# Performance work log

Measured on AMD Instinct MI355X. Metric: run time of the kernel, lower is better.

## Reference

```python
import jax, jax.numpy as jnp
import numpy as np

N_NODES = 50000
BN_EPS = 1e-5


def setup_inputs() -> dict:
    key = jax.random.key(0)
    ks = jax.random.split(key, 10)
    n, e, d, L = N_NODES, 500000, 128, 2
    x = jax.random.normal(ks[0], (n, d), dtype=jnp.float32)
    edge_index = jax.random.randint(ks[1], (2, e), 0, n, dtype=jnp.int64)
    edge_attr = jax.random.normal(ks[2], (e, d), dtype=jnp.float32)
    W1 = jax.random.normal(ks[3], (L, d, d), dtype=jnp.float32) * 0.05
    b1 = jax.random.normal(ks[4], (L, d), dtype=jnp.float32) * 0.02
    gamma = 1.0 + 0.1 * jax.random.normal(ks[5], (L, d), dtype=jnp.float32)
    beta = 0.1 * jax.random.normal(ks[6], (L, d), dtype=jnp.float32)
    W2 = jax.random.normal(ks[7], (L, d, d), dtype=jnp.float32) * 0.05
    b2 = jax.random.normal(ks[8], (L, d), dtype=jnp.float32) * 0.02
    return {"x": x, "edge_index": edge_index, "edge_attr": edge_attr,
            "W1": W1, "b1": b1, "gamma": gamma, "beta": beta, "W2": W2, "b2": b2}


def _gine_layer(x, src, dst, edge_attr, W1l, b1l, gl, bl, W2l, b2l):
    # GINEConv message: relu(x_j + edge_attr), sum-aggregated to target nodes
    msg = jax.nn.relu(x[src] + edge_attr)              # [E, d]
    agg = jax.ops.segment_sum(msg, dst, num_segments=N_NODES)  # [N, d]
    h = (x + agg) @ W1l + b1l                           # eps=0 -> (1+eps)*x = x
    # BatchNorm1d over nodes (train-mode batch stats, biased var)
    mu = jnp.mean(h, axis=0)
    var = jnp.mean(jnp.square(h - mu), axis=0)
    h = (h - mu) * jax.lax.rsqrt(var + BN_EPS) * gl + bl
    h = jax.nn.relu(h)
    h = jax.nn.relu(h @ W2l + b2l)
    return jax.nn.relu(h)  # encoder's outer activation


def reference(x, edge_index, edge_attr, W1, b1, gamma, beta, W2, b2):
    src, dst = edge_index[0], edge_index[1]
    L = W1.shape[0]
    for l in range(L):
        x = _gine_layer(x, src, dst, edge_attr, W1[l], b1[l], gamma[l], beta[l], W2[l], b2[l])
    return x
```

## Files before the change

kernel.cpp:

```cpp
#include <hip/hip_runtime.h>

#define BN_EPS 1e-5f

using f4 = __attribute__((ext_vector_type(4))) float;

__device__ inline f4 relu4(f4 v) {
    v.x = fmaxf(v.x, 0.f); v.y = fmaxf(v.y, 0.f);
    v.z = fmaxf(v.z, 0.f); v.w = fmaxf(v.w, 0.f);
    return v;
}

__global__ __launch_bounds__(256) void detect_i64_kernel(const int* __restrict__ ei,
                                                         int* __restrict__ flag, int npairs,
                                                         int* __restrict__ deg, int N) {
    __shared__ int ok;
    if (threadIdx.x == 0) ok = 1;
    __syncthreads();
    bool bad = false;
    for (int i = threadIdx.x; i < npairs; i += 256)
        bad |= (ei[2 * i + 1] != 0);
    if (bad) ok = 0;
    int nq = N >> 2;
    int4* d4 = (int4*)deg;
    for (int i = threadIdx.x; i < nq; i += 256) d4[i] = make_int4(0, 0, 0, 0);
    for (int i = (nq << 2) + threadIdx.x; i < N; i += 256) deg[i] = 0;
    __syncthreads();
    if (threadIdx.x == 0) *flag = ok;
}

__global__ __launch_bounds__(256) void canon_kernel(const int* __restrict__ ei,
                                                    const int* __restrict__ flag,
                                                    int* __restrict__ canon,
                                                    int* __restrict__ deg, int n2, int E) {
    int i = blockIdx.x * 256 + threadIdx.x;
    if (i >= n2) return;
    int wide = *flag;
    int v = wide ? ei[2 * i] : ei[i];
    canon[i] = v;
    if (i >= E) atomicAdd(&deg[v], 1);
}

__global__ __launch_bounds__(256) void scan_blk_kernel(const int* __restrict__ deg,
                                                       int* __restrict__ rowptr,
                                                       int* __restrict__ partials, int N) {
    __shared__ int s[256];
    int b = blockIdx.x, t = threadIdx.x;
    int base = b * 1024 + t * 4;
    int4 v = make_int4(0, 0, 0, 0);
    if (base + 3 < N) v = *(const int4*)(deg + base);
    else {
        if (base < N) v.x = deg[base];
        if (base + 1 < N) v.y = deg[base + 1];
        if (base + 2 < N) v.z = deg[base + 2];
        if (base + 3 < N) v.w = deg[base + 3];
    }
    s[t] = v.x + v.y + v.z + v.w;
    __syncthreads();
    for (int off = 1; off < 256; off <<= 1) {
        int u = (t >= off) ? s[t - off] : 0;
        __syncthreads();
        s[t] += u;
        __syncthreads();
    }
    int excl = (t == 0) ? 0 : s[t - 1];
    int4 w;
    w.x = excl;
    w.y = excl + v.x;
    w.z = w.y + v.y;
    w.w = w.z + v.z;
    if (base + 3 < N) *(int4*)(rowptr + base) = w;
    else {
        if (base < N) rowptr[base] = w.x;
        if (base + 1 < N) rowptr[base + 1] = w.y;
        if (base + 2 < N) rowptr[base + 2] = w.z;
        if (base + 3 < N) rowptr[base + 3] = w.w;
    }
    if (t == 255) partials[b] = s[255];
}

__global__ __launch_bounds__(256) void scan_part_kernel(int* __restrict__ partials, int nb) {
    __shared__ int s[256];
    int t = threadIdx.x;
    if (nb <= 256) {
        s[t] = (t < nb) ? partials[t] : 0;
        __syncthreads();
        for (int off = 1; off < 256; off <<= 1) {
            int u = (t >= off) ? s[t - off] : 0;
            __syncthreads();
            s[t] += u;
            __syncthreads();
        }
        if (t < nb) partials[t] = (t == 0) ? 0 : s[t - 1];
    } else if (t == 0) {
        int run = 0;
        for (int i = 0; i < nb; ++i) { int d = partials[i]; partials[i] = run; run += d; }
    }
}

__global__ __launch_bounds__(256) void scan_add_kernel(int* __restrict__ rowptr,
                                                       int* __restrict__ cursor,
                                                       const int* __restrict__ partials,
                                                       int N, int E) {
    int i = blockIdx.x * 256 + threadIdx.x;
    if (i < N) {
        int v = rowptr[i] + partials[i >> 10];
        rowptr[i] = v;
        cursor[i] = v;
    }
    if (i == N) rowptr[N] = E;
}

__global__ __launch_bounds__(256) void fill_kernel(const int* __restrict__ src,
                                                   const int* __restrict__ dst,
                                                   int* __restrict__ cursor,
                                                   int2* __restrict__ pbuf, int E) {
    int e = blockIdx.x * 256 + threadIdx.x;
    if (e >= E) return;
    int d = dst[e];
    int pos = atomicAdd(&cursor[d], 1);
    pbuf[pos] = make_int2(e, src[e]);
}

__global__ __launch_bounds__(256) void gather_kernel(const float* __restrict__ x,
                                                     const float* __restrict__ ea,
                                                     const int* __restrict__ rowptr,
                                                     const int2* __restrict__ pbuf,
                                                     float* __restrict__ aggx,
                                                     float* __restrict__ sums, int N) {
    if (blockIdx.x == 0) sums[threadIdx.x] = 0.f;
    int t = blockIdx.x * 256 + threadIdx.x;
    int n = t >> 5;
    if (n >= N) return;
    int f = t & 31;
    int lo = rowptr[n], hi = rowptr[n + 1];
    f4 acc0 = ((const f4*)(x + (size_t)n * 128))[f];
    f4 acc1 = {0.f, 0.f, 0.f, 0.f};
    f4 acc2 = {0.f, 0.f, 0.f, 0.f};
    f4 acc3 = {0.f, 0.f, 0.f, 0.f};
    int i = lo;
    for (; i + 4 <= hi; i += 4) {
        int2 q0 = pbuf[i];
        int2 q1 = pbuf[i + 1];
        int2 q2 = pbuf[i + 2];
        int2 q3 = pbuf[i + 3];
        f4 xa = ((const f4*)(x + (size_t)q0.y * 128))[f];
        f4 aa = __builtin_nontemporal_load(((const f4*)(ea + (size_t)q0.x * 128)) + f);
        f4 xb = ((const f4*)(x + (size_t)q1.y * 128))[f];
        f4 ab = __builtin_nontemporal_load(((const f4*)(ea + (size_t)q1.x * 128)) + f);
        f4 xc = ((const f4*)(x + (size_t)q2.y * 128))[f];
        f4 ac = __builtin_nontemporal_load(((const f4*)(ea + (size_t)q2.x * 128)) + f);
        f4 xd = ((const f4*)(x + (size_t)q3.y * 128))[f];
        f4 ad = __builtin_nontemporal_load(((const f4*)(ea + (size_t)q3.x * 128)) + f);
        acc0 += relu4(xa + aa);
        acc1 += relu4(xb + ab);
        acc2 += relu4(xc + ac);
        acc3 += relu4(xd + ad);
    }
    for (; i + 2 <= hi; i += 2) {
        int2 q0 = pbuf[i];
        int2 q1 = pbuf[i + 1];
        f4 xa = ((const f4*)(x + (size_t)q0.y * 128))[f];
        f4 aa = __builtin_nontemporal_load(((const f4*)(ea + (size_t)q0.x * 128)) + f);
        f4 xb = ((const f4*)(x + (size_t)q1.y * 128))[f];
        f4 ab = __builtin_nontemporal_load(((const f4*)(ea + (size_t)q1.x * 128)) + f);
        acc0 += relu4(xa + aa);
        acc1 += relu4(xb + ab);
    }
    if (i < hi) {
        int2 q0 = pbuf[i];
        f4 xa = ((const f4*)(x + (size_t)q0.y * 128))[f];
        f4 aa = __builtin_nontemporal_load(((const f4*)(ea + (size_t)q0.x * 128)) + f);
        acc0 += relu4(xa + aa);
    }
    f4 r = (acc0 + acc1) + (acc2 + acc3);
    ((f4*)(aggx + (size_t)n * 128))[f] = r;
}

template <int MODE>
__global__ __launch_bounds__(256) void gemm_kernel(const float* __restrict__ A,
                                                   const float* __restrict__ W,
                                                   const float* __restrict__ bias,
                                                   float* __restrict__ sums,
                                                   const float* __restrict__ gamma,
                                                   const float* __restrict__ beta,
                                                   float* __restrict__ out, int N,
                                                   float invN) {
    __shared__ float sA[64][132];
    __shared__ float sW[32][128];
    __shared__ float sScale[128];
    __shared__ float sShift[128];
    int t = threadIdx.x;
    int rbase = blockIdx.x * 64;

    if (MODE == 2) {
        if (t < 128) {
            float mean = sums[t] * invN;
            float var = sums[128 + t] * invN - mean * mean;
            float inv = rsqrtf(var + BN_EPS);
            float sc = gamma[t] * inv;
            sScale[t] = sc;
            sShift[t] = beta[t] - mean * sc;
        }
        __syncthreads();
    }

    {
        int colq = t & 31;
        int r0 = t >> 5;
        float4 s4 = make_float4(0.f, 0.f, 0.f, 0.f), sh4 = make_float4(0.f, 0.f, 0.f, 0.f);
        if (MODE == 2) {
            s4 = reinterpret_cast<const float4*>(sScale)[colq];
            sh4 = reinterpret_cast<const float4*>(sShift)[colq];
        }
#pragma unroll
        for (int it = 0; it < 8; ++it) {
            int r = r0 + it * 8;
            int row = rbase + r;
            float4 v = make_float4(0.f, 0.f, 0.f, 0.f);
            if (row < N) {
                float4 a = reinterpret_cast<const float4*>(A + (size_t)row * 128)[colq];
                if (MODE == 1) {
                    v = a;
                } else {
                    v.x = fmaxf(a.x * s4.x + sh4.x, 0.f);
                    v.y = fmaxf(a.y * s4.y + sh4.y, 0.f);
                    v.z = fmaxf(a.z * s4.z + sh4.z, 0.f);
                    v.w = fmaxf(a.w * s4.w + sh4.w, 0.f);
                }
            }
            *reinterpret_cast<float4*>(&sA[r][colq * 4]) = v;
        }
    }

    float acc[4][8];
#pragma unroll
    for (int r = 0; r < 4; ++r)
#pragma unroll
        for (int c = 0; c < 8; ++c) acc[r][c] = 0.f;

    int cg = t & 15, rg = t >> 4;
    int c0a = cg * 4;
    int c0b = 64 + cg * 4;

    for (int kc = 0; kc < 4; ++kc) {
        __syncthreads();
#pragma unroll
        for (int pass = 0; pass < 4; ++pass) {
            int kk = (t >> 5) + pass * 8;
            int k = kc * 32 + kk;
            float4 w = reinterpret_cast<const float4*>(W + (size_t)k * 128)[t & 31];
            *reinterpret_cast<float4*>(&sW[kk][(t & 31) * 4]) = w;
        }
        __syncthreads();
#pragma unroll
        for (int kk0 = 0; kk0 < 32; kk0 += 4) {
            float4 a[4];
#pragma unroll
            for (int r = 0; r < 4; ++r)
                a[r] = *reinterpret_cast<const float4*>(&sA[rg * 4 + r][kc * 32 + kk0]);
#pragma unroll
            for (int j = 0; j < 4; ++j) {
                float4 w0 = *reinterpret_cast<const float4*>(&sW[kk0 + j][c0a]);
                float4 w1 = *reinterpret_cast<const float4*>(&sW[kk0 + j][c0b]);
#pragma unroll
                for (int r = 0; r < 4; ++r) {
                    float av = (j == 0) ? a[r].x : (j == 1) ? a[r].y : (j == 2) ? a[r].z : a[r].w;
                    acc[r][0] += av * w0.x;
                    acc[r][1] += av * w0.y;
                    acc[r][2] += av * w0.z;
                    acc[r][3] += av * w0.w;
                    acc[r][4] += av * w1.x;
                    acc[r][5] += av * w1.y;
                    acc[r][6] += av * w1.z;
                    acc[r][7] += av * w1.w;
                }
            }
        }
    }

    float4 b0 = *reinterpret_cast<const float4*>(bias + c0a);
    float4 b1v = *reinterpret_cast<const float4*>(bias + c0b);
    float cs[8], cs2[8];
#pragma unroll
    for (int j = 0; j < 8; ++j) { cs[j] = 0.f; cs2[j] = 0.f; }

#pragma unroll
    for (int r = 0; r < 4; ++r) {
        int row = rbase + rg * 4 + r;
        if (row >= N) continue;
        float4 o0, o1;
        o0.x = acc[r][0] + b0.x;  o0.y = acc[r][1] + b0.y;
        o0.z = acc[r][2] + b0.z;  o0.w = acc[r][3] + b0.w;
        o1.x = acc[r][4] + b1v.x; o1.y = acc[r][5] + b1v.y;
        o1.z = acc[r][6] + b1v.z; o1.w = acc[r][7] + b1v.w;
        if (MODE == 2) {
            o0.x = fmaxf(o0.x, 0.f); o0.y = fmaxf(o0.y, 0.f);
            o0.z = fmaxf(o0.z, 0.f); o0.w = fmaxf(o0.w, 0.f);
            o1.x = fmaxf(o1.x, 0.f); o1.y = fmaxf(o1.y, 0.f);
            o1.z = fmaxf(o1.z, 0.f); o1.w = fmaxf(o1.w, 0.f);
        } else {
            cs[0] += o0.x; cs2[0] += o0.x * o0.x;
            cs[1] += o0.y; cs2[1] += o0.y * o0.y;
            cs[2] += o0.z; cs2[2] += o0.z * o0.z;
            cs[3] += o0.w; cs2[3] += o0.w * o0.w;
            cs[4] += o1.x; cs2[4] += o1.x * o1.x;
            cs[5] += o1.y; cs2[5] += o1.y * o1.y;
            cs[6] += o1.z; cs2[6] += o1.z * o1.z;
            cs[7] += o1.w; cs2[7] += o1.w * o1.w;
        }
        *reinterpret_cast<float4*>(out + (size_t)row * 128 + c0a) = o0;
        *reinterpret_cast<float4*>(out + (size_t)row * 128 + c0b) = o1;
    }

    if (MODE == 1) {
        __syncthreads();
        float* red = &sA[0][0];
        float* red2 = red + 2048;
        int base = (rg * 16 + cg) * 8;
#pragma unroll
        for (int j = 0; j < 8; ++j) { red[base + j] = cs[j]; red2[base + j] = cs2[j]; }
        __syncthreads();
        if (t < 128) {
            int cgj = (t & 63) >> 2;
            int j = (t & 3) + ((t >> 6) << 2);
            float s = 0.f, s2 = 0.f;
#pragma unroll
            for (int rr = 0; rr < 16; ++rr) {
                s += red[(rr * 16 + cgj) * 8 + j];
                s2 += red2[(rr * 16 + cgj) * 8 + j];
            }
            unsafeAtomicAdd(&sums[t], s);
            unsafeAtomicAdd(&sums[128 + t], s2);
        }
    }
}

extern "C" void kernel_launch(void* const* d_in, const int* in_sizes, int n_in,
                              void* d_out, int out_size, void* d_ws, size_t ws_size,
                              hipStream_t stream) {
    const float* x     = (const float*)d_in[0];
    const int*   ei    = (const int*)d_in[1];
    const float* ea    = (const float*)d_in[2];
    const float* W1    = (const float*)d_in[3];
    const float* b1    = (const float*)d_in[4];
    const float* gamma = (const float*)d_in[5];
    const float* beta  = (const float*)d_in[6];
    const float* W2    = (const float*)d_in[7];
    const float* b2    = (const float*)d_in[8];

    int N = in_sizes[0] / 128;
    int E = in_sizes[2] / 128;
    int L = in_sizes[3] / (128 * 128);

    size_t NF = (size_t)N * 128;
    float* aggx  = (float*)d_ws;
    float* h     = aggx + NF;
    float* sums  = h + NF;
    int*   canon  = (int*)(sums + 256);
    int*   deg    = canon + (size_t)2 * E;
    int*   rowptr = deg + N;
    int*   cursor = rowptr + N + 2;
    int2*  pbuf   = (int2*)(cursor + N);
    int*   partials = (int*)(pbuf + E);
    int*   flag   = partials + ((N + 1023) / 1024) + 1;

    int npairs = (E < 4096) ? E : 4096;
    detect_i64_kernel<<<1, 256, 0, stream>>>(ei, flag, npairs, deg, N);
    int E2 = 2 * E;
    canon_kernel<<<(E2 + 255) / 256, 256, 0, stream>>>(ei, flag, canon, deg, E2, E);
    const int* src = canon;
    const int* dst = canon + E;

    int nb = (N + 1023) / 1024;
    scan_blk_kernel<<<nb, 256, 0, stream>>>(deg, rowptr, partials, N);
    scan_part_kernel<<<1, 256, 0, stream>>>(partials, nb);
    scan_add_kernel<<<(N + 256) / 256, 256, 0, stream>>>(rowptr, cursor, partials, N, E);
    int eBlocks = (E + 255) / 256;
    fill_kernel<<<eBlocks, 256, 0, stream>>>(src, dst, cursor, pbuf, E);

    int gatherBlocks = (N * 32 + 255) / 256;
    int gemmBlocks = (N + 63) / 64;
    float invN = 1.0f / (float)N;
    const float* xin = x;
    for (int l = 0; l < L; ++l) {
        float* xout = (float*)d_out;
        gather_kernel<<<gatherBlocks, 256, 0, stream>>>(xin, ea, rowptr, pbuf, aggx, sums, N);
        gemm_kernel<1><<<gemmBlocks, 256, 0, stream>>>(aggx, W1 + (size_t)l * 16384,
                                                       b1 + (size_t)l * 128, sums,
                                                       nullptr, nullptr, h, N, invN);
        gemm_kernel<2><<<gemmBlocks, 256, 0, stream>>>(h, W2 + (size_t)l * 16384,
                                                       b2 + (size_t)l * 128, sums,
                                                       gamma + (size_t)l * 128,
                                                       beta + (size_t)l * 128, xout, N, invN);
        xin = xout;
    }
}
```

Baseline: 677.3 us.

## Fuse gather into first GEMM and cache edge features as fp16 in CSR order

Merges the neighbour gather/aggregation into the first GEMM kernel so aggregated rows go straight into shared memory instead of a global aggx buffer. Layer 0 also writes edge_attr converted to fp16 in CSR-sorted order, so later layers stream half the bytes sequentially instead of gathering fp32 rows at random. Per-layer BN sums are zeroed once in the scan kernel. The fp16 edge copy loses precision in later layers, and the fused gather runs with only 64 rows per block, which may reduce memory-level parallelism.

```diff
diff --git a/kernel.cpp b/kernel.cpp
--- a/kernel.cpp
+++ b/kernel.cpp
@@ -3,6 +3,7 @@
 #define BN_EPS 1e-5f
 
 using f4 = __attribute__((ext_vector_type(4))) float;
+using h4 = __attribute__((ext_vector_type(4))) _Float16;
 
 __device__ inline f4 relu4(f4 v) {
     v.x = fmaxf(v.x, 0.f); v.y = fmaxf(v.y, 0.f);
@@ -100,8 +101,10 @@
 __global__ __launch_bounds__(256) void scan_add_kernel(int* __restrict__ rowptr,
                                                        int* __restrict__ cursor,
                                                        const int* __restrict__ partials,
+                                                       float* __restrict__ sums, int nsum,
                                                        int N, int E) {
     int i = blockIdx.x * 256 + threadIdx.x;
+    if (i < nsum) sums[i] = 0.f;
     if (i < N) {
         int v = rowptr[i] + partials[i >> 10];
         rowptr[i] = v;
@@ -121,115 +124,99 @@
     pbuf[pos] = make_int2(e, src[e]);
 }
 
-__global__ __launch_bounds__(256) void gather_kernel(const float* __restrict__ x,
-                                                     const float* __restrict__ ea,
-                                                     const int* __restrict__ rowptr,
-                                                     const int2* __restrict__ pbuf,
-                                                     float* __restrict__ aggx,
-                                                     float* __restrict__ sums, int N) {
-    if (blockIdx.x == 0) sums[threadIdx.x] = 0.f;
-    int t = blockIdx.x * 256 + threadIdx.x;
-    int n = t >> 5;
-    if (n >= N) return;
-    int f = t & 31;
-    int lo = rowptr[n], hi = rowptr[n + 1];
-    f4 acc0 = ((const f4*)(x + (size_t)n * 128))[f];
-    f4 acc1 = {0.f, 0.f, 0.f, 0.f};
-    f4 acc2 = {0.f, 0.f, 0.f, 0.f};
-    f4 acc3 = {0.f, 0.f, 0.f, 0.f};
-    int i = lo;
-    for (; i + 4 <= hi; i += 4) {
-        int2 q0 = pbuf[i];
-        int2 q1 = pbuf[i + 1];
-        int2 q2 = pbuf[i + 2];
-        int2 q3 = pbuf[i + 3];
-        f4 xa = ((const f4*)(x + (size_t)q0.y * 128))[f];
-        f4 aa = __builtin_nontemporal_load(((const f4*)(ea + (size_t)q0.x * 128)) + f);
-        f4 xb = ((const f4*)(x + (size_t)q1.y * 128))[f];
-        f4 ab = __builtin_nontemporal_load(((const f4*)(ea + (size_t)q1.x * 128)) + f);
-        f4 xc = ((const f4*)(x + (size_t)q2.y * 128))[f];
-        f4 ac = __builtin_nontemporal_load(((const f4*)(ea + (size_t)q2.x * 128)) + f);
-        f4 xd = ((const f4*)(x + (size_t)q3.y * 128))[f];
-        f4 ad = __builtin_nontemporal_load(((const f4*)(ea + (size_t)q3.x * 128)) + f);
-        acc0 += relu4(xa + aa);
-        acc1 += relu4(xb + ab);
-        acc2 += relu4(xc + ac);
-        acc3 += relu4(xd + ad);
-    }
-    for (; i + 2 <= hi; i += 2) {
-        int2 q0 = pbuf[i];
-        int2 q1 = pbuf[i + 1];
-        f4 xa = ((const f4*)(x + (size_t)q0.y * 128))[f];
-        f4 aa = __builtin_nontemporal_load(((const f4*)(ea + (size_t)q0.x * 128)) + f);
-        f4 xb = ((const f4*)(x + (size_t)q1.y * 128))[f];
-        f4 ab = __builtin_nontemporal_load(((const f4*)(ea + (size_t)q1.x * 128)) + f);
-        acc0 += relu4(xa + aa);
-        acc1 += relu4(xb + ab);
-    }
-    if (i < hi) {
-        int2 q0 = pbuf[i];
-        f4 xa = ((const f4*)(x + (size_t)q0.y * 128))[f];
-        f4 aa = __builtin_nontemporal_load(((const f4*)(ea + (size_t)q0.x * 128)) + f);
-        acc0 += relu4(xa + aa);
-    }
-    f4 r = (acc0 + acc1) + (acc2 + acc3);
-    ((f4*)(aggx + (size_t)n * 128))[f] = r;
-}
-
-template <int MODE>
-__global__ __launch_bounds__(256) void gemm_kernel(const float* __restrict__ A,
-                                                   const float* __restrict__ W,
-                                                   const float* __restrict__ bias,
-                                                   float* __restrict__ sums,
-                                                   const float* __restrict__ gamma,
-                                                   const float* __restrict__ beta,
-                                                   float* __restrict__ out, int N,
-                                                   float invN) {
+template <int EAH>
+__global__ __launch_bounds__(256) void gg1_kernel(const float* __restrict__ x,
+                                                  const float* __restrict__ ea,
+                                                  _Float16* __restrict__ eah,
+                                                  const int* __restrict__ rowptr,
+                                                  const int2* __restrict__ pbuf,
+                                                  const float* __restrict__ W,
+                                                  const float* __restrict__ bias,
+                                                  float* __restrict__ sums,
+                                                  float* __restrict__ out, int N) {
     __shared__ float sA[64][132];
     __shared__ float sW[32][128];
-    __shared__ float sScale[128];
-    __shared__ float sShift[128];
     int t = threadIdx.x;
     int rbase = blockIdx.x * 64;
-
-    if (MODE == 2) {
-        if (t < 128) {
-            float mean = sums[t] * invN;
-            float var = sums[128 + t] * invN - mean * mean;
-            float inv = rsqrtf(var + BN_EPS);
-            float sc = gamma[t] * inv;
-            sScale[t] = sc;
-            sShift[t] = beta[t] - mean * sc;
-        }
-        __syncthreads();
-    }
-
-    {
-        int colq = t & 31;
-        int r0 = t >> 5;
-        float4 s4 = make_float4(0.f, 0.f, 0.f, 0.f), sh4 = make_float4(0.f, 0.f, 0.f, 0.f);
-        if (MODE == 2) {
-            s4 = reinterpret_cast<const float4*>(sScale)[colq];
-            sh4 = reinterpret_cast<const float4*>(sShift)[colq];
-        }
-#pragma unroll
-        for (int it = 0; it < 8; ++it) {
-            int r = r0 + it * 8;
-            int row = rbase + r;
-            float4 v = make_float4(0.f, 0.f, 0.f, 0.f);
-            if (row < N) {
-                float4 a = reinterpret_cast<const float4*>(A + (size_t)row * 128)[colq];
-                if (MODE == 1) {
-                    v = a;
-                } else {
-                    v.x = fmaxf(a.x * s4.x + sh4.x, 0.f);
-                    v.y = fmaxf(a.y * s4.y + sh4.y, 0.f);
-                    v.z = fmaxf(a.z * s4.z + sh4.z, 0.f);
-                    v.w = fmaxf(a.w * s4.w + sh4.w, 0.f);
+    int f = t & 31, g = t >> 5;
+
+    for (int it = 0; it < 8; ++it) {
+        int r = g * 8 + it;
+        int n = rbase + r;
+        f4 acc0 = {0.f, 0.f, 0.f, 0.f};
+        f4 acc1 = {0.f, 0.f, 0.f, 0.f};
+        f4 acc2 = {0.f, 0.f, 0.f, 0.f};
+        f4 acc3 = {0.f, 0.f, 0.f, 0.f};
+        if (n < N) {
+            acc0 = ((const f4*)(x + (size_t)n * 128))[f];
+            int lo = rowptr[n], hi = rowptr[n + 1];
+            int i = lo;
+            if (EAH == 1) {
+                const h4* ep = (const h4*)eah;
+                for (; i + 4 <= hi; i += 4) {
+                    int2 q0 = pbuf[i];
+                    int2 q1 = pbuf[i + 1];
+                    int2 q2 = pbuf[i + 2];
+                    int2 q3 = pbuf[i + 3];
+                    f4 xa = ((const f4*)(x + (size_t)q0.y * 128))[f];
+                    h4 ha = __builtin_nontemporal_load(ep + (size_t)i * 32 + f);
+                    f4 xb = ((const f4*)(x + (size_t)q1.y * 128))[f];
+                    h4 hb = __builtin_nontemporal_load(ep + (size_t)(i + 1) * 32 + f);
+                    f4 xc = ((const f4*)(x + (size_t)q2.y * 128))[f];
+                    h4 hc = __builtin_nontemporal_load(ep + (size_t)(i + 2) * 32 + f);
+                    f4 xd = ((const f4*)(x + (size_t)q3.y * 128))[f];
+                    h4 hd = __builtin_nontemporal_load(ep + (size_t)(i + 3) * 32 + f);
+                    acc0 += relu4(xa + __builtin_convertvector(ha, f4));
+                    acc1 += relu4(xb + __builtin_convertvector(hb, f4));
+                    acc2 += relu4(xc + __builtin_convertvector(hc, f4));
+                    acc3 += relu4(xd + __builtin_convertvector(hd, f4));
+                }
+                for (; i < hi; ++i) {
+                    int2 q0 = pbuf[i];
+                    f4 xa = ((const f4*)(x + (size_t)q0.y * 128))[f];
+                    h4 ha = __builtin_nontemporal_load(ep + (size_t)i * 32 + f);
+                    acc0 += relu4(xa + __builtin_convertvector(ha, f4));
+                }
+            } else {
+                for (; i + 4 <= hi; i += 4) {
+                    int2 q0 = pbuf[i];
+                    int2 q1 = pbuf[i + 1];
+                    int2 q2 = pbuf[i + 2];
+                    int2 q3 = pbuf[i + 3];
+                    f4 xa = ((const f4*)(x + (size_t)q0.y * 128))[f];
+                    f4 aa = __builtin_nontemporal_load(((const f4*)(ea + (size_t)q0.x * 128)) + f);
+                    f4 xb = ((const f4*)(x + (size_t)q1.y * 128))[f];
+                    f4 ab = __builtin_nontemporal_load(((const f4*)(ea + (size_t)q1.x * 128)) + f);
+                    f4 xc = ((const f4*)(x + (size_t)q2.y * 128))[f];
+                    f4 ac = __builtin_nontemporal_load(((const f4*)(ea + (size_t)q2.x * 128)) + f);
+                    f4 xd = ((const f4*)(x + (size_t)q3.y * 128))[f];
+                    f4 ad = __builtin_nontemporal_load(((const f4*)(ea + (size_t)q3.x * 128)) + f);
+                    if (EAH == 0) {
+                        h4* ep = (h4*)eah;
+                        __builtin_nontemporal_store(__builtin_convertvector(aa, h4), ep + (size_t)i * 32 + f);
+                        __builtin_nontemporal_store(__builtin_convertvector(ab, h4), ep + (size_t)(i + 1) * 32 + f);
+                        __builtin_nontemporal_store(__builtin_convertvector(ac, h4), ep + (size_t)(i + 2) * 32 + f);
+                        __builtin_nontemporal_store(__builtin_convertvector(ad, h4), ep + (size_t)(i + 3) * 32 + f);
+                    }
+                    acc0 += relu4(xa + aa);
+                    acc1 += relu4(xb + ab);
+                    acc2 += relu4(xc + ac);
+                    acc3 += relu4(xd + ad);
+                }
+                for (; i < hi; ++i) {
+                    int2 q0 = pbuf[i];
+                    f4 xa = ((const f4*)(x + (size_t)q0.y * 128))[f];
+                    f4 aa = __builtin_nontemporal_load(((const f4*)(ea + (size_t)q0.x * 128)) + f);
+                    if (EAH == 0) {
+                        h4* ep = (h4*)eah;
+                        __builtin_nontemporal_store(__builtin_convertvector(aa, h4), ep + (size_t)i * 32 + f);
+                    }
+                    acc0 += relu4(xa + aa);
                 }
             }
-            *reinterpret_cast<float4*>(&sA[r][colq * 4]) = v;
-        }
+        }
+        f4 rv = (acc0 + acc1) + (acc2 + acc3);
+        *(f4*)&sA[r][f * 4] = rv;
     }
 
     float acc[4][8];
@@ -293,45 +280,144 @@
         o0.z = acc[r][2] + b0.z;  o0.w = acc[r][3] + b0.w;
         o1.x = acc[r][4] + b1v.x; o1.y = acc[r][5] + b1v.y;
         o1.z = acc[r][6] + b1v.z; o1.w = acc[r][7] + b1v.w;
-        if (MODE == 2) {
-            o0.x = fmaxf(o0.x, 0.f); o0.y = fmaxf(o0.y, 0.f);
-            o0.z = fmaxf(o0.z, 0.f); o0.w = fmaxf(o0.w, 0.f);
-            o1.x = fmaxf(o1.x, 0.f); o1.y = fmaxf(o1.y, 0.f);
-            o1.z = fmaxf(o1.z, 0.f); o1.w = fmaxf(o1.w, 0.f);
-        } else {
-            cs[0] += o0.x; cs2[0] += o0.x * o0.x;
-            cs[1] += o0.y; cs2[1] += o0.y * o0.y;
-            cs[2] += o0.z; cs2[2] += o0.z * o0.z;
-            cs[3] += o0.w; cs2[3] += o0.w * o0.w;
-            cs[4] += o1.x; cs2[4] += o1.x * o1.x;
-            cs[5] += o1.y; cs2[5] += o1.y * o1.y;
-            cs[6] += o1.z; cs2[6] += o1.z * o1.z;
-            cs[7] += o1.w; cs2[7] += o1.w * o1.w;
-        }
+        cs[0] += o0.x; cs2[0] += o0.x * o0.x;
+        cs[1] += o0.y; cs2[1] += o0.y * o0.y;
+        cs[2] += o0.z; cs2[2] += o0.z * o0.z;
+        cs[3] += o0.w; cs2[3] += o0.w * o0.w;
+        cs[4] += o1.x; cs2[4] += o1.x * o1.x;
+        cs[5] += o1.y; cs2[5] += o1.y * o1.y;
+        cs[6] += o1.z; cs2[6] += o1.z * o1.z;
+        cs[7] += o1.w; cs2[7] += o1.w * o1.w;
         *reinterpret_cast<float4*>(out + (size_t)row * 128 + c0a) = o0;
         *reinterpret_cast<float4*>(out + (size_t)row * 128 + c0b) = o1;
     }
 
-    if (MODE == 1) {
-        __syncthreads();
-        float* red = &sA[0][0];
-        float* red2 = red + 2048;
-        int base = (rg * 16 + cg) * 8;
-#pragma unroll
-        for (int j = 0; j < 8; ++j) { red[base + j] = cs[j]; red2[base + j] = cs2[j]; }
-        __syncthreads();
-        if (t < 128) {
-            int cgj = (t & 63) >> 2;
-            int j = (t & 3) + ((t >> 6) << 2);
-            float s = 0.f, s2 = 0.f;
-#pragma unroll
-            for (int rr = 0; rr < 16; ++rr) {
-                s += red[(rr * 16 + cgj) * 8 + j];
-                s2 += red2[(rr * 16 + cgj) * 8 + j];
+    __syncthreads();
+    float* red = &sA[0][0];
+    float* red2 = red + 2048;
+    int base = (rg * 16 + cg) * 8;
+#pragma unroll
+    for (int j = 0; j < 8; ++j) { red[base + j] = cs[j]; red2[base + j] = cs2[j]; }
+    __syncthreads();
+    if (t < 128) {
+        int cgj = (t & 63) >> 2;
+        int j = (t & 3) + ((t >> 6) << 2);
+        float s = 0.f, s2 = 0.f;
+#pragma unroll
+        for (int rr = 0; rr < 16; ++rr) {
+            s += red[(rr * 16 + cgj) * 8 + j];
+            s2 += red2[(rr * 16 + cgj) * 8 + j];
+        }
+        unsafeAtomicAdd(&sums[t], s);
+        unsafeAtomicAdd(&sums[128 + t], s2);
+    }
+}
+
+__global__ __launch_bounds__(256) void gemm2_kernel(const float* __restrict__ A,
+                                                    const float* __restrict__ W,
+                                                    const float* __restrict__ bias,
+                                                    const float* __restrict__ sums,
+                                                    const float* __restrict__ gamma,
+                                                    const float* __restrict__ beta,
+                                                    float* __restrict__ out, int N,
+                                                    float invN) {
+    __shared__ float sA[64][132];
+    __shared__ float sW[32][128];
+    __shared__ float sScale[128];
+    __shared__ float sShift[128];
+    int t = threadIdx.x;
+    int rbase = blockIdx.x * 64;
+
+    if (t < 128) {
+        float mean = sums[t] * invN;
+        float var = sums[128 + t] * invN - mean * mean;
+        float inv = rsqrtf(var + BN_EPS);
+        float sc = gamma[t] * inv;
+        sScale[t] = sc;
+        sShift[t] = beta[t] - mean * sc;
+    }
+    __syncthreads();
+
+    {
+        int colq = t & 31;
+        int r0 = t >> 5;
+        float4 s4 = reinterpret_cast<const float4*>(sScale)[colq];
+        float4 sh4 = reinterpret_cast<const float4*>(sShift)[colq];
+#pragma unroll
+        for (int it = 0; it < 8; ++it) {
+            int r = r0 + it * 8;
+            int row = rbase + r;
+            float4 v = make_float4(0.f, 0.f, 0.f, 0.f);
+            if (row < N) {
+                float4 a = reinterpret_cast<const float4*>(A + (size_t)row * 128)[colq];
+                v.x = fmaxf(a.x * s4.x + sh4.x, 0.f);
+                v.y = fmaxf(a.y * s4.y + sh4.y, 0.f);
+                v.z = fmaxf(a.z * s4.z + sh4.z, 0.f);
+                v.w = fmaxf(a.w * s4.w + sh4.w, 0.f);
             }
-            unsafeAtomicAdd(&sums[t], s);
-            unsafeAtomicAdd(&sums[128 + t], s2);
-        }
+            *reinterpret_cast<float4*>(&sA[r][colq * 4]) = v;
+        }
+    }
+
+    float acc[4][8];
+#pragma unroll
+    for (int r = 0; r < 4; ++r)
+#pragma unroll
+        for (int c = 0; c < 8; ++c) acc[r][c] = 0.f;
+
+    int cg = t & 15, rg = t >> 4;
+    int c0a = cg * 4;
+    int c0b = 64 + cg * 4;
+
+    for (int kc = 0; kc < 4; ++kc) {
+        __syncthreads();
+#pragma unroll
+        for (int pass = 0; pass < 4; ++pass) {
+            int kk = (t >> 5) + pass * 8;
+            int k = kc * 32 + kk;
+            float4 w = reinterpret_cast<const float4*>(W + (size_t)k * 128)[t & 31];
+            *reinterpret_cast<float4*>(&sW[kk][(t & 31) * 4]) = w;
+        }
+        __syncthreads();
+#pragma unroll
+        for (int kk0 = 0; kk0 < 32; kk0 += 4) {
+            float4 a[4];
+#pragma unroll
+            for (int r = 0; r < 4; ++r)
+                a[r] = *reinterpret_cast<const float4*>(&sA[rg * 4 + r][kc * 32 + kk0]);
+#pragma unroll
+            for (int j = 0; j < 4; ++j) {
+                float4 w0 = *reinterpret_cast<const float4*>(&sW[kk0 + j][c0a]);
+                float4 w1 = *reinterpret_cast<const float4*>(&sW[kk0 + j][c0b]);
+#pragma unroll
+                for (int r = 0; r < 4; ++r) {
+                    float av = (j == 0) ? a[r].x : (j == 1) ? a[r].y : (j == 2) ? a[r].z : a[r].w;
+                    acc[r][0] += av * w0.x;
+                    acc[r][1] += av * w0.y;
+                    acc[r][2] += av * w0.z;
+                    acc[r][3] += av * w0.w;
+                    acc[r][4] += av * w1.x;
+                    acc[r][5] += av * w1.y;
+                    acc[r][6] += av * w1.z;
+                    acc[r][7] += av * w1.w;
+                }
+            }
+        }
+    }
+
+    float4 b0 = *reinterpret_cast<const float4*>(bias + c0a);
+    float4 b1v = *reinterpret_cast<const float4*>(bias + c0b);
+#pragma unroll
+    for (int r = 0; r < 4; ++r) {
+        int row = rbase + rg * 4 + r;
+        if (row >= N) continue;
+        float4 o0, o1;
+        o0.x = fmaxf(acc[r][0] + b0.x, 0.f);  o0.y = fmaxf(acc[r][1] + b0.y, 0.f);
+        o0.z = fmaxf(acc[r][2] + b0.z, 0.f);  o0.w = fmaxf(acc[r][3] + b0.w, 0.f);
+        o1.x = fmaxf(acc[r][4] + b1v.x, 0.f); o1.y = fmaxf(acc[r][5] + b1v.y, 0.f);
+        o1.z = fmaxf(acc[r][6] + b1v.z, 0.f); o1.w = fmaxf(acc[r][7] + b1v.w, 0.f);
+        *reinterpret_cast<float4*>(out + (size_t)row * 128 + c0a) = o0;
+        *reinterpret_cast<float4*>(out + (size_t)row * 128 + c0b) = o1;
     }
 }
 
@@ -353,16 +439,16 @@
     int L = in_sizes[3] / (128 * 128);
 
     size_t NF = (size_t)N * 128;
-    float* aggx  = (float*)d_ws;
-    float* h     = aggx + NF;
-    float* sums  = h + NF;
-    int*   canon  = (int*)(sums + 256);
-    int*   deg    = canon + (size_t)2 * E;
-    int*   rowptr = deg + N;
-    int*   cursor = rowptr + N + 2;
-    int2*  pbuf   = (int2*)(cursor + N);
-    int*   partials = (int*)(pbuf + E);
-    int*   flag   = partials + ((N + 1023) / 1024) + 1;
+    float*     h      = (float*)d_ws;
+    float*     sums   = h + NF;
+    _Float16*  eah    = (_Float16*)(sums + 256 * L);
+    int*       canon  = (int*)(eah + (size_t)E * 128);
+    int*       deg    = canon + (size_t)2 * E;
+    int*       rowptr = deg + N;
+    int*       cursor = rowptr + N + 2;
+    int2*      pbuf   = (int2*)(cursor + N);
+    int*       partials = (int*)(pbuf + E);
+    int*       flag   = partials + ((N + 1023) / 1024) + 1;
 
     int npairs = (E < 4096) ? E : 4096;
     detect_i64_kernel<<<1, 256, 0, stream>>>(ei, flag, npairs, deg, N);
@@ -374,24 +460,34 @@
     int nb = (N + 1023) / 1024;
     scan_blk_kernel<<<nb, 256, 0, stream>>>(deg, rowptr, partials, N);
     scan_part_kernel<<<1, 256, 0, stream>>>(partials, nb);
-    scan_add_kernel<<<(N + 256) / 256, 256, 0, stream>>>(rowptr, cursor, partials, N, E);
+    scan_add_kernel<<<(N + 256) / 256, 256, 0, stream>>>(rowptr, cursor, partials,
+                                                         sums, 256 * L, N, E);
     int eBlocks = (E + 255) / 256;
     fill_kernel<<<eBlocks, 256, 0, stream>>>(src, dst, cursor, pbuf, E);
 
-    int gatherBlocks = (N * 32 + 255) / 256;
     int gemmBlocks = (N + 63) / 64;
     float invN = 1.0f / (float)N;
     const float* xin = x;
     for (int l = 0; l < L; ++l) {
         float* xout = (float*)d_out;
-        gather_kernel<<<gatherBlocks, 256, 0, stream>>>(xin, ea, rowptr, pbuf, aggx, sums, N);
-        gemm_kernel<1><<<gemmBlocks, 256, 0, stream>>>(aggx, W1 + (size_t)l * 16384,
-                                                       b1 + (size_t)l * 128, sums,
-                                                       nullptr, nullptr, h, N, invN);
-        gemm_kernel<2><<<gemmBlocks, 256, 0, stream>>>(h, W2 + (size_t)l * 16384,
-                                                       b2 + (size_t)l * 128, sums,
-                                                       gamma + (size_t)l * 128,
-                                                       beta + (size_t)l * 128, xout, N, invN);
+        const float* W1l = W1 + (size_t)l * 16384;
+        const float* b1l = b1 + (size_t)l * 128;
+        float* sums_l = sums + (size_t)l * 256;
+        if (l == 0) {
+            if (L > 1)
+                gg1_kernel<0><<<gemmBlocks, 256, 0, stream>>>(xin, ea, eah, rowptr, pbuf,
+                                                              W1l, b1l, sums_l, h, N);
+            else
+                gg1_kernel<2><<<gemmBlocks, 256, 0, stream>>>(xin, ea, eah, rowptr, pbuf,
+                                                              W1l, b1l, sums_l, h, N);
+        } else {
+            gg1_kernel<1><<<gemmBlocks, 256, 0, stream>>>(xin, ea, eah, rowptr, pbuf,
+                                                          W1l, b1l, sums_l, h, N);
+        }
+        gemm2_kernel<<<gemmBlocks, 256, 0, stream>>>(h, W2 + (size_t)l * 16384,
+                                                     b2 + (size_t)l * 128, sums_l,
+                                                     gamma + (size_t)l * 128,
+                                                     beta + (size_t)l * 128, xout, N, invN);
         xin = xout;
     }
 }
```

New measurement: 708.1 us. 4.6% more time.
